# Performance work log

Measured on AMD Instinct MI355X. Metric: run time of the kernel, lower is better.

Reference implementation:

```python
import jax, jax.numpy as jnp
import numpy as np

H = 16          # num_attention_heads
DH = 64         # attention_head_size = hidden // heads
WINDOW = 128    # window_size
GLOBAL_RATIO = 0.1
SCALE = 1.0 / np.sqrt(DH)


def _combined_mask(seq_len):
    # sliding window: |i-j| <= window_size // 2
    pos = jnp.arange(seq_len)
    dist = pos[None, :] - pos[:, None]
    window_mask = jnp.abs(dist) <= (WINDOW // 2)
    # global tokens: first max(1, int(S * ratio)) positions, full row+col
    num_global = max(1, int(seq_len * GLOBAL_RATIO))
    is_global = pos < num_global
    global_mask = is_global[:, None] | is_global[None, :]
    return window_mask | global_mask  # [S, S] bool


def setup_inputs() -> dict:
    key = jax.random.key(0)
    ks = jax.random.split(key, 9)
    B, S, Dm = 2, 2048, 1024
    s = 0.02
    return {
        "hidden_states": jax.random.normal(ks[0], (B, S, Dm), jnp.float32),
        "Wq": jax.random.normal(ks[1], (Dm, Dm), jnp.float32) * s,
        "bq": jax.random.normal(ks[2], (Dm,), jnp.float32) * s,
        "Wk": jax.random.normal(ks[3], (Dm, Dm), jnp.float32) * s,
        "bk": jax.random.normal(ks[4], (Dm,), jnp.float32) * s,
        "Wv": jax.random.normal(ks[5], (Dm, Dm), jnp.float32) * s,
        "bv": jax.random.normal(ks[6], (Dm,), jnp.float32) * s,
        "Wo": jax.random.normal(ks[7], (Dm, Dm), jnp.float32) * s,
        "bo": jax.random.normal(ks[8], (Dm,), jnp.float32) * s,
    }


def reference(hidden_states, Wq, bq, Wk, bk, Wv, bv, Wo, bo):
    B, S, Dm = hidden_states.shape

    def heads(x):  # [B,S,Dm] -> [B,H,S,Dh]
        return x.reshape(B, S, H, DH).transpose(0, 2, 1, 3)

    q = heads(hidden_states @ Wq.T + bq)
    k = heads(hidden_states @ Wk.T + bk)
    v = heads(hidden_states @ Wv.T + bv)

    scores = jnp.einsum("bhqd,bhkd->bhqk", q, k) * SCALE
    mask = _combined_mask(S)  # [S,S] bool, True = attend
    scores = scores + jnp.where(mask, 0.0, -10000.0)[None, None]

    probs = jax.nn.softmax(scores, axis=-1)
    ctx = jnp.einsum("bhqk,bhkd->bhqd", probs, v)
    ctx = ctx.transpose(0, 2, 1, 3).reshape(B, S, Dm)
    return ctx @ Wo.T + bo
```

## Files before the change

### kernel.cpp

```cpp
#include <hip/hip_runtime.h>


#define B_   2
#define S_   2048
#define DM   1024
#define H_   16
#define NG   204
#define BS_  4096
#define SCL2 0.1803368801111204f
#define NEGF -3.0e38f

typedef unsigned short u16;
typedef unsigned int   u32;
typedef __attribute__((ext_vector_type(8))) short frag8;
typedef __attribute__((ext_vector_type(4))) short frag4;
typedef __attribute__((ext_vector_type(4))) float f32x4;

#define MFMA16(A, Bf, C) __builtin_amdgcn_mfma_f32_16x16x32_bf16((A), (Bf), (C), 0, 0, 0)

__device__ __forceinline__ f32x4 mfma_16x16x16_bf16(frag4 a, frag4 b, f32x4 c) {
#if defined(__HIP_DEVICE_COMPILE__)
  return __builtin_amdgcn_mfma_f32_16x16x16bf16_1k(a, b, c, 0, 0, 0);
#else
  (void)a; (void)b;
  return c;
#endif
}

#define GLD16(g, l)                                                              \
  __builtin_amdgcn_global_load_lds((const __attribute__((address_space(1))) u32*)(g), \
                                   (__attribute__((address_space(3))) u32*)(l), 16, 0, 0)
#define EXP2(x) exp2f(x)

__device__ __forceinline__ u16 f2bf(float f) {
  union { float f; u32 u; } c; c.f = f;
  u32 u = c.u + 0x7fffu + ((c.u >> 16) & 1u);
  return (u16)(u >> 16);
}
__device__ __forceinline__ u16 f2bfc(float f) {
  union { float f; u32 u; } c; c.f = f;
  return (u16)((c.u + 0x8000u) >> 16);
}

__global__ void cvt_all(const float* __restrict__ X,  const float* __restrict__ Wq,
                        const float* __restrict__ Wk, const float* __restrict__ Wv,
                        const float* __restrict__ Wo,
                        u16* Xb, u16* Wqb, u16* Wkb, u16* Wvb, u16* Wob) {
  const int chunk = blockIdx.y;
  const float* src; u16* dst;
  if (chunk < 4)      { src = X + (size_t)chunk * 1048576; dst = Xb + (size_t)chunk * 1048576; }
  else if (chunk == 4){ src = Wq; dst = Wqb; }
  else if (chunk == 5){ src = Wk; dst = Wkb; }
  else if (chunk == 6){ src = Wv; dst = Wvb; }
  else                { src = Wo; dst = Wob; }
  int i = blockIdx.x * 256 + threadIdx.x;
  float4 v = ((const float4*)src)[i];
  u32 lo = (u32)f2bf(v.x) | ((u32)f2bf(v.y) << 16);
  u32 hi = (u32)f2bf(v.z) | ((u32)f2bf(v.w) << 16);
  ((uint2*)dst)[i] = make_uint2(lo, hi);
}

__device__ __forceinline__ void gemm_mainloop(const u16* __restrict__ A, const u16* __restrict__ Bm,
                                              int bm, int bn, u16* As, u16* Bs,
                                              f32x4 acc[4][4]) {
  const int tid = threadIdx.x;
  const int wv = tid >> 6, lane = tid & 63, l15 = lane & 15, quad = lane >> 4;
  const int wm = wv & 1, wn = wv >> 1;

  const u16* gA[4]; const u16* gB[4];
#pragma unroll
  for (int c = 0; c < 4; ++c) {
    int idx = (wv * 4 + c) * 64 + lane;
    int r = idx >> 3;
    int cb = (idx & 7) ^ (r & 7);
    gA[c] = A  + (size_t)(bm + r) * DM + cb * 8;
    gB[c] = Bm + (size_t)(bn + r) * DM + cb * 8;
  }

  int offA[4][2], offB[4][2];
#pragma unroll
  for (int i = 0; i < 4; ++i)
#pragma unroll
    for (int h = 0; h < 2; ++h) {
      int mA = wm * 64 + i * 16 + l15;
      int mB = wn * 64 + i * 16 + l15;
      int cb = (quad + h * 4) ^ (l15 & 7);
      offA[i][h] = ((mA << 3) + cb) << 4;
      offB[i][h] = ((mB << 3) + cb) << 4;
    }

  for (int k0 = 0; k0 < DM; k0 += 64) {
#pragma unroll
    for (int c = 0; c < 4; ++c) {
      GLD16(gA[c] + k0, (char*)As + (wv * 4 + c) * 1024);
      GLD16(gB[c] + k0, (char*)Bs + (wv * 4 + c) * 1024);
    }
    __syncthreads();
    frag8 af[4][2], bf[4][2];
#pragma unroll
    for (int i = 0; i < 4; ++i) {
      af[i][0] = *(const frag8*)((const char*)As + offA[i][0]);
      af[i][1] = *(const frag8*)((const char*)As + offA[i][1]);
      bf[i][0] = *(const frag8*)((const char*)Bs + offB[i][0]);
      bf[i][1] = *(const frag8*)((const char*)Bs + offB[i][1]);
    }
#pragma unroll
    for (int h = 0; h < 2; ++h)
#pragma unroll
      for (int i = 0; i < 4; ++i)
#pragma unroll
        for (int j = 0; j < 4; ++j)
          acc[i][j] = MFMA16(af[i][h], bf[j][h], acc[i][j]);
    __syncthreads();
  }
}

__global__ __launch_bounds__(256, 3) void gemm_qkv(const u16* __restrict__ Xb,
    const u16* __restrict__ Wqb, const u16* __restrict__ Wkb, const u16* __restrict__ Wvb,
    const float* __restrict__ bq, const float* __restrict__ bk, const float* __restrict__ bv,
    u16* __restrict__ Qb, u16* __restrict__ Kb, u16* __restrict__ Vt) {
  __shared__ u16 As[8192], Bs[8192];
  const int bm = blockIdx.y * 128;
  const int which = blockIdx.x >> 3;
  const int bnl = (blockIdx.x & 7) * 128;
  const u16* W = (which == 0) ? Wqb : (which == 1) ? Wkb : Wvb;
  const float* bias = (which == 0) ? bq : (which == 1) ? bk : bv;

  f32x4 acc[4][4] = {};
  gemm_mainloop(Xb, W, bm, bnl, As, Bs, acc);

  const int tid = threadIdx.x, wv = tid >> 6, lane = tid & 63, l15 = lane & 15, quad = lane >> 4;
  const int wm = wv & 1, wn = wv >> 1;
  if (which < 2) {
    u16* O = (which == 0) ? Qb : Kb;
    const float scl = (which == 0) ? SCL2 : 1.0f;
#pragma unroll
    for (int j = 0; j < 4; ++j) {
      int col = bnl + wn * 64 + j * 16 + l15;
      float bb = bias[col];
#pragma unroll
      for (int i = 0; i < 4; ++i) {
        int row0 = bm + wm * 64 + i * 16 + quad * 4;
#pragma unroll
        for (int r = 0; r < 4; ++r)
          O[(size_t)(row0 + r) * DM + col] = f2bf((acc[i][j][r] + bb) * scl);
      }
    }
  } else {
#pragma unroll
    for (int j = 0; j < 4; ++j) {
      int col = bnl + wn * 64 + j * 16 + l15;
      float bb = bias[col];
#pragma unroll
      for (int i = 0; i < 4; ++i) {
        int row0 = bm + wm * 64 + i * 16 + quad * 4;
        u32 lo = (u32)f2bf(acc[i][j][0] + bb) | ((u32)f2bf(acc[i][j][1] + bb) << 16);
        u32 hi = (u32)f2bf(acc[i][j][2] + bb) | ((u32)f2bf(acc[i][j][3] + bb) << 16);
        *(uint2*)&Vt[(size_t)col * BS_ + row0] = make_uint2(lo, hi);
      }
    }
  }
}

__global__ __launch_bounds__(256, 3) void gemm_wo(const u16* __restrict__ Cx,
    const u16* __restrict__ Wob, const float* __restrict__ bo, float* __restrict__ out) {
  __shared__ u16 As[4096], Bs[8192];
  const int tid = threadIdx.x;
  const int wv = tid >> 6, lane = tid & 63, l15 = lane & 15, quad = lane >> 4;
  const int bm = blockIdx.y * 64, bn = blockIdx.x * 128;

  const u16* gA[2]; const u16* gB[4];
  int ldsA[2], ldsB[4];
#pragma unroll
  for (int c = 0; c < 2; ++c) {
    int slot = c * 256 + wv * 64 + lane;
    int r = slot >> 3, cb = (slot & 7) ^ (r & 7);
    gA[c] = Cx + (size_t)(bm + r) * DM + cb * 8;
    ldsA[c] = (c * 256 + wv * 64) * 16;
  }
#pragma unroll
  for (int c = 0; c < 4; ++c) {
    int slot = c * 256 + wv * 64 + lane;
    int r = slot >> 3, cb = (slot & 7) ^ (r & 7);
    gB[c] = Wob + (size_t)(bn + r) * DM + cb * 8;
    ldsB[c] = (c * 256 + wv * 64) * 16;
  }

  int offA[2], offB[8][2];
#pragma unroll
  for (int h = 0; h < 2; ++h) {
    int rowA = wv * 16 + l15;
    offA[h] = ((rowA << 3) + ((quad + h * 4) ^ (l15 & 7))) << 4;
#pragma unroll
    for (int j = 0; j < 8; ++j) {
      int rowB = j * 16 + l15;
      offB[j][h] = ((rowB << 3) + ((quad + h * 4) ^ (l15 & 7))) << 4;
    }
  }

  f32x4 acc[8] = {};
  for (int k0 = 0; k0 < DM; k0 += 64) {
#pragma unroll
    for (int c = 0; c < 2; ++c) GLD16(gA[c] + k0, (char*)As + ldsA[c]);
#pragma unroll
    for (int c = 0; c < 4; ++c) GLD16(gB[c] + k0, (char*)Bs + ldsB[c]);
    __syncthreads();
    frag8 af0 = *(const frag8*)((const char*)As + offA[0]);
    frag8 af1 = *(const frag8*)((const char*)As + offA[1]);
#pragma unroll
    for (int j = 0; j < 8; ++j) {
      frag8 bf0 = *(const frag8*)((const char*)Bs + offB[j][0]);
      frag8 bf1 = *(const frag8*)((const char*)Bs + offB[j][1]);
      acc[j] = MFMA16(af0, bf0, acc[j]);
      acc[j] = MFMA16(af1, bf1, acc[j]);
    }
    __syncthreads();
  }

#pragma unroll
  for (int j = 0; j < 8; ++j) {
    int col = bn + j * 16 + l15;
    float bb = bo[col];
    int row0 = bm + wv * 16 + quad * 4;
#pragma unroll
    for (int r = 0; r < 4; ++r)
      out[(size_t)(row0 + r) * DM + col] = acc[j][r] + bb;
  }
}

__global__ __launch_bounds__(256) void attn_kernel(const u16* __restrict__ Q,
                                                   const u16* __restrict__ K,
                                                   const u16* __restrict__ Vt,
                                                   u16* __restrict__ Ctx,
                                                   float* __restrict__ Op,
                                                   float* __restrict__ Lp) {
  __shared__ u16 Ks[2][4096];
  __shared__ u16 Vs[2][4096];

  const int tid = threadIdx.x, w = tid >> 6, lane = tid & 63, l15 = lane & 15, quad = lane >> 4;
  const int blk = blockIdx.x;
  const int bh = blk & 31, unit = blk >> 5;
  const int b = bh >> 4, h = bh & 15;
  const bool heavy = unit < 16;
  const int strip = heavy ? (unit >> 2) : (unit - 12);
  const int q0 = strip * 64;
  const int qw = q0 + w * 16;

  const u16* qrow = Q + (size_t)(b * S_ + qw + l15) * DM + h * 64;
  frag8 bq0 = *(const frag8*)(qrow + quad * 8);
  frag8 bq1 = *(const frag8*)(qrow + quad * 8 + 32);

  const u16* gK[2]; const u16* gV[2]; int ldso[2];
#pragma unroll
  for (int c = 0; c < 2; ++c) {
    int sl = (w * 2 + c) * 64 + lane;
    int r = sl >> 3;
    int fr = (r & 7) ^ (((r >> 3) & 1) << 2);
    int cb = (sl & 7) ^ fr;
    gK[c] = K  + (size_t)(b * S_ + r) * DM + h * 64 + cb * 8;
    gV[c] = Vt + (size_t)(h * 64 + r) * BS_ + (size_t)b * S_ + cb * 8;
    ldso[c] = (w * 2 + c) * 1024;
  }

  const int fl = (l15 & 7) ^ (((l15 >> 3) & 1) << 2);
  int offKb[2];
#pragma unroll
  for (int hh = 0; hh < 2; ++hh)
    offKb[hh] = ((l15 << 3) + ((quad + hh * 4) ^ fl)) << 4;
  int offVb[4];
#pragma unroll
  for (int kg = 0; kg < 4; ++kg)
    offVb[kg] = ((((l15 << 3) + ((((kg << 1) | (quad >> 1))) ^ fl)) << 4)
                 | ((quad & 1) << 3));

  const int qidx = qw + l15;
  const bool qglob = qidx < NG;
  const frag4 ones = {(short)0x3F80, (short)0x3F80, (short)0x3F80, (short)0x3F80};

  f32x4 o[4] = {};
  f32x4 o_l = {};

  auto stage = [&](int t, int buf) {
#pragma unroll
    for (int c = 0; c < 2; ++c) {
      GLD16(gK[c] + (size_t)t * 64 * DM, (char*)Ks[buf] + ldso[c]);
      GLD16(gV[c] + t * 64,              (char*)Vs[buf] + ldso[c]);
    }
  };

  auto step = [&](int kt, int p, bool domask) {
    const char* kb_ = (const char*)Ks[p];
    const char* vb_ = (const char*)Vs[p];
    f32x4 st[4] = {};
#pragma unroll
    for (int kg = 0; kg < 4; ++kg) {
      frag8 ak0 = *(const frag8*)(kb_ + offKb[0] + kg * 2048);
      frag8 ak1 = *(const frag8*)(kb_ + offKb[1] + kg * 2048);
      st[kg] = MFMA16(ak0, bq0, st[kg]);
      st[kg] = MFMA16(ak1, bq1, st[kg]);
    }
    const int k0 = kt * 64;
    frag4 pk[4];
    if (domask) {
#pragma unroll
      for (int kg = 0; kg < 4; ++kg) {
        float pr[4];
#pragma unroll
        for (int r = 0; r < 4; ++r) {
          int kc = k0 + kg * 16 + quad * 4 + r;
          int d = qidx - kc;
          bool act = ((unsigned)(d + 64) <= 128u) || qglob || (kc < NG);
          pr[r] = EXP2(act ? st[kg][r] : NEGF);
        }
        pk[kg] = frag4{(short)f2bfc(pr[0]), (short)f2bfc(pr[1]),
                       (short)f2bfc(pr[2]), (short)f2bfc(pr[3])};
      }
    } else {
#pragma unroll
      for (int kg = 0; kg < 4; ++kg) {
        float pr[4];
#pragma unroll
        for (int r = 0; r < 4; ++r) pr[r] = EXP2(st[kg][r]);
        pk[kg] = frag4{(short)f2bfc(pr[0]), (short)f2bfc(pr[1]),
                       (short)f2bfc(pr[2]), (short)f2bfc(pr[3])};
      }
    }
#pragma unroll
    for (int kg = 0; kg < 4; ++kg) {
      o_l = mfma_16x16x16_bf16(ones, pk[kg], o_l);
#pragma unroll
      for (int nt = 0; nt < 4; ++nt) {
        frag4 av = *(const frag4*)(vb_ + offVb[kg] + nt * 2048);
        o[nt] = mfma_16x16x16_bf16(av, pk[kg], o[nt]);
      }
    }
  };

  if (heavy) {
    const int seg = unit & 3;
    const int kt0 = seg * 8;
    const bool dm = (strip == 3);
    int p = 0;
    stage(kt0, 0);
#pragma unroll 1
    for (int tt = 0; tt < 8; ++tt) {
      __syncthreads();
      if (tt < 7) stage(kt0 + tt + 1, p ^ 1);
      step(kt0 + tt, p, dm && (kt0 + tt > 2));
      p ^= 1;
    }
    float* op = Op + ((size_t)((bh * 4 + strip) * 4 + seg)) * 4096;
    float* lp = Lp + ((size_t)((bh * 4 + strip) * 4 + seg)) * 64;
    if (quad == 0) lp[w * 16 + l15] = o_l[0];
#pragma unroll
    for (int nt = 0; nt < 4; ++nt)
      *(float4*)&op[(w * 16 + l15) * 64 + nt * 16 + quad * 4] =
          make_float4(o[nt][0], o[nt][1], o[nt][2], o[nt][3]);
    return;
  }

  auto activef = [&](int t) {
    int k0 = t * 64;
    return (k0 < NG) || (k0 + 63 >= q0 - 64 && k0 <= q0 + 127);
  };
  auto nextt = [&](int cur) { int n = cur + 1; while (n < 32 && !activef(n)) ++n; return n; };

  int kt = 0, p = 0;
  stage(0, 0);
  for (;;) {
    int ktn = nextt(kt);
    bool more = ktn < 32;
    __syncthreads();
    if (more) stage(ktn, p ^ 1);
    step(kt, p, kt > 2);
    if (!more) break;
    kt = ktn; p ^= 1;
  }

  float inv = 1.0f / o_l[0];
  u16* crow = Ctx + (size_t)((size_t)b * S_ + qw + l15) * DM + h * 64;
#pragma unroll
  for (int nt = 0; nt < 4; ++nt) {
    u32 lo = (u32)f2bf(o[nt][0] * inv) | ((u32)f2bf(o[nt][1] * inv) << 16);
    u32 hi = (u32)f2bf(o[nt][2] * inv) | ((u32)f2bf(o[nt][3] * inv) << 16);
    *(uint2*)&crow[nt * 16 + quad * 4] = make_uint2(lo, hi);
  }
}

__global__ __launch_bounds__(256) void combine_kernel(const float* __restrict__ Op,
                                                      const float* __restrict__ Lp,
                                                      u16* __restrict__ Ctx) {
  const int blk = blockIdx.x;
  const int bh = blk & 31, strip = blk >> 5;
  const int b = bh >> 4, h = bh & 15;
  const int t = threadIdx.x;
  const int row = t >> 2, colg = (t & 3) * 16;

  const float* opb = Op + ((size_t)(bh * 4 + strip) * 4) * 4096;
  const float* lpb = Lp + ((size_t)(bh * 4 + strip) * 4) * 64;

  float l = lpb[row] + lpb[64 + row] + lpb[128 + row] + lpb[192 + row];
  float acc[16];
#pragma unroll
  for (int e = 0; e < 16; ++e) acc[e] = opb[row * 64 + colg + e];
#pragma unroll
  for (int seg = 1; seg < 4; ++seg)
#pragma unroll
    for (int e = 0; e < 16; ++e) acc[e] += opb[seg * 4096 + row * 64 + colg + e];

  float inv = 1.0f / l;
  u32 pk[8];
#pragma unroll
  for (int p = 0; p < 8; ++p)
    pk[p] = (u32)f2bf(acc[2 * p] * inv) | ((u32)f2bf(acc[2 * p + 1] * inv) << 16);
  u16* dst = Ctx + (size_t)((size_t)b * S_ + strip * 64 + row) * DM + h * 64 + colg;
  *(uint4*)dst       = make_uint4(pk[0], pk[1], pk[2], pk[3]);
  *(uint4*)(dst + 8) = make_uint4(pk[4], pk[5], pk[6], pk[7]);
}

extern "C" void kernel_launch(void* const* d_in, const int* in_sizes, int n_in,
                              void* d_out, int out_size, void* d_ws, size_t ws_size,
                              hipStream_t stream) {
  const float* X  = (const float*)d_in[0];
  const float* Wq = (const float*)d_in[1];
  const float* bq = (const float*)d_in[2];
  const float* Wk = (const float*)d_in[3];
  const float* bk = (const float*)d_in[4];
  const float* Wv = (const float*)d_in[5];
  const float* bv = (const float*)d_in[6];
  const float* Wo = (const float*)d_in[7];
  const float* bo = (const float*)d_in[8];
  float* out = (float*)d_out;

  u16* ws = (u16*)d_ws;
  const size_t NX = (size_t)BS_ * DM;
  const size_t NW = (size_t)DM * DM;
  u16* Xb  = ws;
  u16* Wqb = Xb + NX;
  u16* Wkb = Wqb + NW;
  u16* Wvb = Wkb + NW;
  u16* Wob = Wvb + NW;
  u16* Qb  = Wob + NW;
  u16* Kb  = Qb + NX;
  u16* Vt  = Kb + NX;
  u16* Cx  = Vt + NX;
  float* Op = (float*)(Cx + NX);
  float* Lp = Op + (size_t)32 * 4 * 4 * 4096;

  cvt_all<<<dim3(1024, 8), 256, 0, stream>>>(X, Wq, Wk, Wv, Wo, Xb, Wqb, Wkb, Wvb, Wob);
  gemm_qkv<<<dim3(24, 32), 256, 0, stream>>>(Xb, Wqb, Wkb, Wvb, bq, bk, bv, Qb, Kb, Vt);
  attn_kernel<<<44 * 32, 256, 0, stream>>>(Qb, Kb, Vt, Cx, Op, Lp);
  combine_kernel<<<128, 256, 0, stream>>>(Op, Lp, Cx);
  gemm_wo<<<dim3(8, 64), 256, 0, stream>>>(Cx, Wob, bo, out);
}
```

Measured before the change: 169.9 us.

## Process two query groups per wave in attention to reuse K/V tiles

```diff
diff --git a/kernel.cpp b/kernel.cpp
--- a/kernel.cpp
+++ b/kernel.cpp
@@ -228,12 +228,12 @@
   }
 }
 
-__global__ __launch_bounds__(256) void attn_kernel(const u16* __restrict__ Q,
-                                                   const u16* __restrict__ K,
-                                                   const u16* __restrict__ Vt,
-                                                   u16* __restrict__ Ctx,
-                                                   float* __restrict__ Op,
-                                                   float* __restrict__ Lp) {
+__global__ __launch_bounds__(256, 3) void attn_kernel(const u16* __restrict__ Q,
+                                                      const u16* __restrict__ K,
+                                                      const u16* __restrict__ Vt,
+                                                      u16* __restrict__ Ctx,
+                                                      float* __restrict__ Op,
+                                                      float* __restrict__ Lp) {
   __shared__ u16 Ks[2][4096];
   __shared__ u16 Vs[2][4096];
 
@@ -241,14 +241,18 @@
   const int blk = blockIdx.x;
   const int bh = blk & 31, unit = blk >> 5;
   const int b = bh >> 4, h = bh & 15;
-  const bool heavy = unit < 16;
-  const int strip = heavy ? (unit >> 2) : (unit - 12);
-  const int q0 = strip * 64;
+  const bool heavy = unit < 8;
+  const int strip = heavy ? (unit >> 2) : 0;
+  const int q0 = heavy ? strip * 128 : 256 + (unit - 8) * 128;
   const int qw = q0 + w * 16;
 
-  const u16* qrow = Q + (size_t)(b * S_ + qw + l15) * DM + h * 64;
-  frag8 bq0 = *(const frag8*)(qrow + quad * 8);
-  frag8 bq1 = *(const frag8*)(qrow + quad * 8 + 32);
+  frag8 bq[2][2];
+#pragma unroll
+  for (int g = 0; g < 2; ++g) {
+    const u16* qrow = Q + (size_t)(b * S_ + qw + g * 64 + l15) * DM + h * 64;
+    bq[g][0] = *(const frag8*)(qrow + quad * 8);
+    bq[g][1] = *(const frag8*)(qrow + quad * 8 + 32);
+  }
 
   const u16* gK[2]; const u16* gV[2]; int ldso[2];
 #pragma unroll
@@ -273,12 +277,13 @@
     offVb[kg] = ((((l15 << 3) + ((((kg << 1) | (quad >> 1))) ^ fl)) << 4)
                  | ((quad & 1) << 3));
 
-  const int qidx = qw + l15;
-  const bool qglob = qidx < NG;
+  int qidx[2]; bool qglob[2];
+#pragma unroll
+  for (int g = 0; g < 2; ++g) { qidx[g] = qw + g * 64 + l15; qglob[g] = qidx[g] < NG; }
   const frag4 ones = {(short)0x3F80, (short)0x3F80, (short)0x3F80, (short)0x3F80};
 
-  f32x4 o[4] = {};
-  f32x4 o_l = {};
+  f32x4 o[2][4] = {};
+  f32x4 o_l[2] = {};
 
   auto stage = [&](int t, int buf) {
 #pragma unroll
@@ -291,47 +296,56 @@
   auto step = [&](int kt, int p, bool domask) {
     const char* kb_ = (const char*)Ks[p];
     const char* vb_ = (const char*)Vs[p];
-    f32x4 st[4] = {};
+    frag8 ak[4][2];
 #pragma unroll
     for (int kg = 0; kg < 4; ++kg) {
-      frag8 ak0 = *(const frag8*)(kb_ + offKb[0] + kg * 2048);
-      frag8 ak1 = *(const frag8*)(kb_ + offKb[1] + kg * 2048);
-      st[kg] = MFMA16(ak0, bq0, st[kg]);
-      st[kg] = MFMA16(ak1, bq1, st[kg]);
+      ak[kg][0] = *(const frag8*)(kb_ + offKb[0] + kg * 2048);
+      ak[kg][1] = *(const frag8*)(kb_ + offKb[1] + kg * 2048);
     }
     const int k0 = kt * 64;
-    frag4 pk[4];
-    if (domask) {
+    frag4 pk[2][4];
+#pragma unroll
+    for (int g = 0; g < 2; ++g) {
+      f32x4 st[4] = {};
 #pragma unroll
       for (int kg = 0; kg < 4; ++kg) {
-        float pr[4];
-#pragma unroll
-        for (int r = 0; r < 4; ++r) {
-          int kc = k0 + kg * 16 + quad * 4 + r;
-          int d = qidx - kc;
-          bool act = ((unsigned)(d + 64) <= 128u) || qglob || (kc < NG);
-          pr[r] = EXP2(act ? st[kg][r] : NEGF);
+        st[kg] = MFMA16(ak[kg][0], bq[g][0], st[kg]);
+        st[kg] = MFMA16(ak[kg][1], bq[g][1], st[kg]);
+      }
+      if (domask) {
+#pragma unroll
+        for (int kg = 0; kg < 4; ++kg) {
+          float pr[4];
+#pragma unroll
+          for (int r = 0; r < 4; ++r) {
+            int kc = k0 + kg * 16 + quad * 4 + r;
+            int d = qidx[g] - kc;
+            bool act = ((unsigned)(d + 64) <= 128u) || qglob[g] || (kc < NG);
+            pr[r] = EXP2(act ? st[kg][r] : NEGF);
+          }
+          pk[g][kg] = frag4{(short)f2bfc(pr[0]), (short)f2bfc(pr[1]),
+                            (short)f2bfc(pr[2]), (short)f2bfc(pr[3])};
         }
-        pk[kg] = frag4{(short)f2bfc(pr[0]), (short)f2bfc(pr[1]),
-                       (short)f2bfc(pr[2]), (short)f2bfc(pr[3])};
+      } else {
+#pragma unroll
+        for (int kg = 0; kg < 4; ++kg) {
+          float pr[4];
+#pragma unroll
+          for (int r = 0; r < 4; ++r) pr[r] = EXP2(st[kg][r]);
+          pk[g][kg] = frag4{(short)f2bfc(pr[0]), (short)f2bfc(pr[1]),
+                            (short)f2bfc(pr[2]), (short)f2bfc(pr[3])};
+        }
       }
-    } else {
-#pragma unroll
-      for (int kg = 0; kg < 4; ++kg) {
-        float pr[4];
-#pragma unroll
-        for (int r = 0; r < 4; ++r) pr[r] = EXP2(st[kg][r]);
-        pk[kg] = frag4{(short)f2bfc(pr[0]), (short)f2bfc(pr[1]),
-                       (short)f2bfc(pr[2]), (short)f2bfc(pr[3])};
-      }
     }
 #pragma unroll
     for (int kg = 0; kg < 4; ++kg) {
-      o_l = mfma_16x16x16_bf16(ones, pk[kg], o_l);
+      o_l[0] = mfma_16x16x16_bf16(ones, pk[0][kg], o_l[0]);
+      o_l[1] = mfma_16x16x16_bf16(ones, pk[1][kg], o_l[1]);
 #pragma unroll
       for (int nt = 0; nt < 4; ++nt) {
         frag4 av = *(const frag4*)(vb_ + offVb[kg] + nt * 2048);
-        o[nt] = mfma_16x16x16_bf16(av, pk[kg], o[nt]);
+        o[0][nt] = mfma_16x16x16_bf16(av, pk[0][kg], o[0][nt]);
+        o[1][nt] = mfma_16x16x16_bf16(av, pk[1][kg], o[1][nt]);
       }
     }
   };
@@ -339,7 +353,7 @@
   if (heavy) {
     const int seg = unit & 3;
     const int kt0 = seg * 8;
-    const bool dm = (strip == 3);
+    const bool dm = (strip == 1);
     int p = 0;
     stage(kt0, 0);
 #pragma unroll 1
@@ -349,19 +363,23 @@
       step(kt0 + tt, p, dm && (kt0 + tt > 2));
       p ^= 1;
     }
-    float* op = Op + ((size_t)((bh * 4 + strip) * 4 + seg)) * 4096;
-    float* lp = Lp + ((size_t)((bh * 4 + strip) * 4 + seg)) * 64;
-    if (quad == 0) lp[w * 16 + l15] = o_l[0];
-#pragma unroll
-    for (int nt = 0; nt < 4; ++nt)
-      *(float4*)&op[(w * 16 + l15) * 64 + nt * 16 + quad * 4] =
-          make_float4(o[nt][0], o[nt][1], o[nt][2], o[nt][3]);
+    float* op = Op + ((size_t)((bh * 2 + strip) * 4 + seg)) * 8192;
+    float* lp = Lp + ((size_t)((bh * 2 + strip) * 4 + seg)) * 128;
+#pragma unroll
+    for (int g = 0; g < 2; ++g) {
+      int rl = g * 64 + w * 16 + l15;
+      if (quad == 0) lp[rl] = o_l[g][0];
+#pragma unroll
+      for (int nt = 0; nt < 4; ++nt)
+        *(float4*)&op[rl * 64 + nt * 16 + quad * 4] =
+            make_float4(o[g][nt][0], o[g][nt][1], o[g][nt][2], o[g][nt][3]);
+    }
     return;
   }
 
   auto activef = [&](int t) {
     int k0 = t * 64;
-    return (k0 < NG) || (k0 + 63 >= q0 - 64 && k0 <= q0 + 127);
+    return (k0 < NG) || (k0 + 63 >= q0 - 64 && k0 <= q0 + 127 + 64);
   };
   auto nextt = [&](int cur) { int n = cur + 1; while (n < 32 && !activef(n)) ++n; return n; };
 
@@ -377,13 +395,16 @@
     kt = ktn; p ^= 1;
   }
 
-  float inv = 1.0f / o_l[0];
-  u16* crow = Ctx + (size_t)((size_t)b * S_ + qw + l15) * DM + h * 64;
-#pragma unroll
-  for (int nt = 0; nt < 4; ++nt) {
-    u32 lo = (u32)f2bf(o[nt][0] * inv) | ((u32)f2bf(o[nt][1] * inv) << 16);
-    u32 hi = (u32)f2bf(o[nt][2] * inv) | ((u32)f2bf(o[nt][3] * inv) << 16);
-    *(uint2*)&crow[nt * 16 + quad * 4] = make_uint2(lo, hi);
+#pragma unroll
+  for (int g = 0; g < 2; ++g) {
+    float inv = 1.0f / o_l[g][0];
+    u16* crow = Ctx + (size_t)((size_t)b * S_ + qw + g * 64 + l15) * DM + h * 64;
+#pragma unroll
+    for (int nt = 0; nt < 4; ++nt) {
+      u32 lo = (u32)f2bf(o[g][nt][0] * inv) | ((u32)f2bf(o[g][nt][1] * inv) << 16);
+      u32 hi = (u32)f2bf(o[g][nt][2] * inv) | ((u32)f2bf(o[g][nt][3] * inv) << 16);
+      *(uint2*)&crow[nt * 16 + quad * 4] = make_uint2(lo, hi);
+    }
   }
 }
 
@@ -391,29 +412,31 @@
                                                       const float* __restrict__ Lp,
                                                       u16* __restrict__ Ctx) {
   const int blk = blockIdx.x;
-  const int bh = blk & 31, strip = blk >> 5;
+  const int bh = blk & 31, s64 = blk >> 5;
   const int b = bh >> 4, h = bh & 15;
   const int t = threadIdx.x;
   const int row = t >> 2, colg = (t & 3) * 16;
-
-  const float* opb = Op + ((size_t)(bh * 4 + strip) * 4) * 4096;
-  const float* lpb = Lp + ((size_t)(bh * 4 + strip) * 4) * 64;
-
-  float l = lpb[row] + lpb[64 + row] + lpb[128 + row] + lpb[192 + row];
+  const int gq = s64 * 64 + row;
+  const int strip = gq >> 7, rIn = gq & 127;
+
+  const float* opb = Op + ((size_t)(bh * 2 + strip) * 4) * 8192;
+  const float* lpb = Lp + ((size_t)(bh * 2 + strip) * 4) * 128;
+
+  float l = lpb[rIn] + lpb[128 + rIn] + lpb[256 + rIn] + lpb[384 + rIn];
   float acc[16];
 #pragma unroll
-  for (int e = 0; e < 16; ++e) acc[e] = opb[row * 64 + colg + e];
+  for (int e = 0; e < 16; ++e) acc[e] = opb[rIn * 64 + colg + e];
 #pragma unroll
   for (int seg = 1; seg < 4; ++seg)
 #pragma unroll
-    for (int e = 0; e < 16; ++e) acc[e] += opb[seg * 4096 + row * 64 + colg + e];
+    for (int e = 0; e < 16; ++e) acc[e] += opb[seg * 8192 + rIn * 64 + colg + e];
 
   float inv = 1.0f / l;
   u32 pk[8];
 #pragma unroll
   for (int p = 0; p < 8; ++p)
     pk[p] = (u32)f2bf(acc[2 * p] * inv) | ((u32)f2bf(acc[2 * p + 1] * inv) << 16);
-  u16* dst = Ctx + (size_t)((size_t)b * S_ + strip * 64 + row) * DM + h * 64 + colg;
+  u16* dst = Ctx + (size_t)((size_t)b * S_ + gq) * DM + h * 64 + colg;
   *(uint4*)dst       = make_uint4(pk[0], pk[1], pk[2], pk[3]);
   *(uint4*)(dst + 8) = make_uint4(pk[4], pk[5], pk[6], pk[7]);
 }
@@ -445,11 +468,11 @@
   u16* Vt  = Kb + NX;
   u16* Cx  = Vt + NX;
   float* Op = (float*)(Cx + NX);
-  float* Lp = Op + (size_t)32 * 4 * 4 * 4096;
+  float* Lp = Op + (size_t)32 * 2 * 4 * 8192;
 
   cvt_all<<<dim3(1024, 8), 256, 0, stream>>>(X, Wq, Wk, Wv, Wo, Xb, Wqb, Wkb, Wvb, Wob);
   gemm_qkv<<<dim3(24, 32), 256, 0, stream>>>(Xb, Wqb, Wkb, Wvb, bq, bk, bv, Qb, Kb, Vt);
-  attn_kernel<<<44 * 32, 256, 0, stream>>>(Qb, Kb, Vt, Cx, Op, Lp);
+  attn_kernel<<<22 * 32, 256, 0, stream>>>(Qb, Kb, Vt, Cx, Op, Lp);
   combine_kernel<<<128, 256, 0, stream>>>(Op, Lp, Cx);
   gemm_wo<<<dim3(8, 64), 256, 0, stream>>>(Cx, Wob, bo, out);
 }
```

Result: no change. 169.6 us (-0.2%).
